# Optimization experiments

Measured on AMD Instinct MI355X. Metric: run time of the kernel, lower is better.

The kernel has to match this reference:

```python
import jax, jax.numpy as jnp
import numpy as np

NUM_ITERS = 2  # quasi-DEER fixed-point iterations (module default num_iters=2)


def _affine_scan(A, b):
    """Parallel first-order linear recurrence h_t = A_t*h_{t-1} + b_t along axis=1.
    A, b: (B, T, H). Equivalent to torch accelerated-scan after removing pow-2 padding."""
    def comb(l, r):
        A1, b1 = l
        A2, b2 = r
        return A2 * A1, A2 * b1 + b2
    return jax.lax.associative_scan(comb, (A, b), axis=1)[1]


def _run_direction(x, W_in, b_in, W_rec, U_z, b_u, num_iters):
    """quasi-DEER evaluation of a MinRNN layer.
    x: (B, T, d_in). Returns states (B, T, H). Initial state h0 = 0 (hx=None)."""
    B, T, _ = x.shape
    H = b_in.shape[0]
    dtype = x.dtype
    h0 = jnp.zeros((B, H), dtype)
    diag_rec = jnp.diagonal(W_rec)  # (H,)
    # z depends only on the input, not on the state -> precompute once.
    z = jnp.tanh(jnp.einsum('bti,hi->bth', x, W_in) + b_in)  # (B, T, H)
    z0, z_rest = z[:, 0], z[:, 1:]
    states = jnp.zeros((B, T, H), dtype)
    for _ in range(num_iters):
        h_prev = states[:, :-1]  # (B, T-1, H), paired with inputs[:,1:]
        u = jax.nn.sigmoid(jnp.einsum('bth,gh->btg', h_prev, W_rec)
                           + jnp.einsum('bth,gh->btg', z_rest, U_z) + b_u)
        fs = u * h_prev + (1.0 - u) * z_rest                      # cell output f
        As = u + (h_prev - z_rest) * u * (1.0 - u) * diag_rec     # diagonal Jacobian
        bs = fs - As * h_prev
        u0 = jax.nn.sigmoid(h0 @ W_rec.T + z0 @ U_z.T + b_u)
        b0 = u0 * h0 + (1.0 - u0) * z0                            # f(x_0, h0)
        A = jnp.concatenate([jnp.zeros_like(b0)[:, None], As], axis=1)  # A0 = 0
        b = jnp.concatenate([b0[:, None], bs], axis=1)
        states = _affine_scan(A, b)
    return states


def _prnn_forward(input, Wf_in, bf_in, Wf_rec, Uf_z, bf_u,
                  Wb_in, bb_in, Wb_rec, Ub_z, bb_u):
    fwd = _run_direction(input, Wf_in, bf_in, Wf_rec, Uf_z, bf_u, NUM_ITERS)
    bwd = _run_direction(input[:, ::-1], Wb_in, bb_in, Wb_rec, Ub_z, bb_u, NUM_ITERS)[:, ::-1]
    output = jnp.concatenate([fwd, bwd], axis=2)      # (B, T, 2H)
    h_n = jnp.stack([fwd[:, -1], bwd[:, 0]])          # (2, B, H)
    return output, h_n


def setup_inputs() -> dict:
    key = jax.random.key(0)
    ks = jax.random.split(key, 12)
    B, T, D_IN, H = 8, 8192, 256, 256
    def minrnn_params(k0, k1, k2, d_in, h):
        kw, kr, ku = k0, k1, k2
        return dict(
            W_in=jax.random.normal(kw, (h, d_in), jnp.float32) / d_in ** 0.5,
            b_in=jnp.zeros((h,), jnp.float32),
            W_rec=jax.random.normal(kr, (h, h), jnp.float32) / h ** 0.5,
            U_z=jax.random.normal(ku, (h, h), jnp.float32) / h ** 0.5,
            b_u=jnp.zeros((h,), jnp.float32),
        )
    pf = minrnn_params(ks[0], ks[1], ks[2], D_IN, H)
    pb = minrnn_params(ks[3], ks[4], ks[5], D_IN, H)
    return {
        'input': jax.random.normal(ks[6], (B, T, D_IN), jnp.float32),
        'Wf_in': pf['W_in'], 'bf_in': pf['b_in'], 'Wf_rec': pf['W_rec'],
        'Uf_z': pf['U_z'], 'bf_u': pf['b_u'],
        'Wb_in': pb['W_in'], 'bb_in': pb['b_in'], 'Wb_rec': pb['W_rec'],
        'Ub_z': pb['U_z'], 'bb_u': pb['b_u'],
    }


def reference(input, Wf_in, bf_in, Wf_rec, Uf_z, bf_u,
              Wb_in, bb_in, Wb_rec, Ub_z, bb_u):
    return _prnn_forward(input, Wf_in, bf_in, Wf_rec, Uf_z, bf_u,
                         Wb_in, bb_in, Wb_rec, Ub_z, bb_u)
```

## Files before the change

### kernel.cpp

```cpp
#include <hip/hip_runtime.h>
#include <stdint.h>

typedef unsigned short u16;
typedef __attribute__((ext_vector_type(8))) short short8v;
typedef __attribute__((ext_vector_type(4))) float f32x4;

#define B_ 8
#define T_ 8192
#define H_ 256
#define M_ 65536
#define MH 16777216
#define NCH 64
#define CHL 128
#define NCHAN 4096

__device__ __forceinline__ u16 f2bf(float f) {
  union { float f; uint32_t u; } v; v.f = f;
  return (u16)((v.u + 0x7FFFu + ((v.u >> 16) & 1u)) >> 16);
}
__device__ __forceinline__ float bf2f(u16 s) {
  union { uint32_t u; float f; } v; v.u = ((uint32_t)s) << 16;
  return v.f;
}
__device__ __forceinline__ float sigm(float x) {
  return __fdividef(1.0f, 1.0f + __expf(-x));
}
__device__ __forceinline__ float tanhfast(float x) {
  return 1.0f - __fdividef(2.0f, __expf(2.0f * x) + 1.0f);
}

__global__ __launch_bounds__(256) void cvt_x_kernel(const float* __restrict__ x,
                                                    u16* __restrict__ xf) {
  size_t i = ((size_t)blockIdx.x * 256 + threadIdx.x) * 8;
  const float4* src = (const float4*)(x + i);
  float4 a = src[0], b = src[1];
  short8v o;
  o[0] = (short)f2bf(a.x); o[1] = (short)f2bf(a.y);
  o[2] = (short)f2bf(a.z); o[3] = (short)f2bf(a.w);
  o[4] = (short)f2bf(b.x); o[5] = (short)f2bf(b.y);
  o[6] = (short)f2bf(b.z); o[7] = (short)f2bf(b.w);
  *(short8v*)(xf + i) = o;
}

__global__ __launch_bounds__(256) void cvt_w_kernel(const float* __restrict__ s0, const float* __restrict__ s1,
                                                    const float* __restrict__ s2, const float* __restrict__ s3,
                                                    const float* __restrict__ s4, const float* __restrict__ s5,
                                                    u16* __restrict__ wbf) {
  int i = blockIdx.x * 256 + threadIdx.x;
  int m = i >> 16, r = i & 65535;
  const float* s = (m == 0) ? s0 : (m == 1) ? s1 : (m == 2) ? s2 : (m == 3) ? s3 : (m == 4) ? s4 : s5;
  wbf[i] = f2bf(s[r]);
}

__device__ __forceinline__ void g2l16(const void* g, void* l) {
  __builtin_amdgcn_global_load_lds((const __attribute__((address_space(1))) void*)g,
                                   (__attribute__((address_space(3))) void*)l, 16, 0, 0);
}

template <int EPI, int REV>
__global__ __launch_bounds__(256) void gemm_k(const u16* __restrict__ A,
                                              const u16* __restrict__ Bw,
                                              const float* __restrict__ bias,
                                              u16* __restrict__ C) {
  __shared__ __align__(16) char ldsA[16384];
  __shared__ __align__(16) char ldsB[16384];
  const int tid = threadIdx.x;
  const int l = tid & 63, w = tid >> 6;
  const int tm = blockIdx.x, tn = blockIdx.y;
  const int m0 = (w >> 1) * 64, n0 = (w & 1) * 64;
  const int wbase = w * 1024;

  f32x4 vzero = {0.f, 0.f, 0.f, 0.f};
  f32x4 acc[4][4];
#pragma unroll
  for (int i = 0; i < 4; ++i)
#pragma unroll
    for (int j = 0; j < 4; ++j) acc[i][j] = vzero;

#pragma unroll
  for (int k0 = 0; k0 < 256; k0 += 64) {
#pragma unroll
    for (int is = 0; is < 4; ++is) {
      const int o = is * 4096 + tid * 16;
      const int row = o >> 7;
      const int cb = o & 127;
      int rA = tm * 128 + row;
      if (REV) { int bb = rA >> 13; int t = rA & 8191; rA = (bb << 13) + (8191 - t); }
      const char* gA = (const char*)A + (size_t)rA * 512 + k0 * 2 + cb;
      g2l16(gA, ldsA + is * 4096 + wbase);
      const int rB = tn * 128 + row;
      const char* gB = (const char*)Bw + (size_t)rB * 512 + k0 * 2 + cb;
      g2l16(gB, ldsB + is * 4096 + wbase);
    }
    __syncthreads();
#pragma unroll
    for (int ks = 0; ks < 2; ++ks) {
      short8v av[4], bv[4];
#pragma unroll
      for (int i = 0; i < 4; ++i) {
        av[i] = *(const short8v*)(ldsA + (m0 + i * 16 + (l & 15)) * 128 + ks * 64 + (l >> 4) * 16);
        bv[i] = *(const short8v*)(ldsB + (n0 + i * 16 + (l & 15)) * 128 + ks * 64 + (l >> 4) * 16);
      }
#pragma unroll
      for (int i = 0; i < 4; ++i)
#pragma unroll
        for (int j = 0; j < 4; ++j)
          acc[i][j] = __builtin_amdgcn_mfma_f32_16x16x32_bf16(av[i], bv[j], acc[i][j], 0, 0, 0);
    }
    __syncthreads();
  }

  const int colb = tn * 128 + n0 + (l & 15);
  const int rowb = tm * 128 + m0 + ((l >> 4) << 2);
#pragma unroll
  for (int j = 0; j < 4; ++j) {
    const int col = colb + j * 16;
    const float bv = (EPI == 2) ? 0.f : bias[col];
#pragma unroll
    for (int i = 0; i < 4; ++i)
#pragma unroll
      for (int r = 0; r < 4; ++r) {
        const int row = rowb + i * 16 + r;
        float xv = acc[i][j][r] + bv;
        if (EPI == 0) xv = tanhfast(xv);
        C[(size_t)row * 256 + col] = f2bf(xv);
      }
  }
}

template <int ITER>
__device__ __forceinline__ void compute_Ab(float zf, float ag, float hp, float dr, bool isT0,
                                           float& Aa, float& bb) {
  const float u = sigm(ag);
  if (isT0) {
    Aa = 0.f; bb = (1.f - u) * zf;
  } else {
    const float g = u * (1.f - u) * dr;
    Aa = u + (hp - zf) * g;
    bb = u * hp + (1.f - u) * zf - Aa * hp;
  }
}

template <int ITER>
__global__ __launch_bounds__(256) void scan_p1_kernel(
    const u16* __restrict__ zb, const u16* __restrict__ zub,
    const u16* __restrict__ s1b, const u16* __restrict__ hw0, const u16* __restrict__ hw1,
    const float* __restrict__ Wf_rec, const float* __restrict__ Wb_rec,
    float* __restrict__ P, float* __restrict__ q) {
  const int wid = blockIdx.x * 4 + (threadIdx.x >> 6);
  const int lane = threadIdx.x & 63;
  const int c = wid & 63;
  int tmp = wid >> 6;
  const int hb = tmp & 3; tmp >>= 2;
  const int b = tmp & 7;
  const int d = tmp >> 3;
  const int h = hb * 64 + lane;
  const float dr = (d ? Wb_rec : Wf_rec)[h * 257];
  const size_t off = ((size_t)b * T_ + (size_t)c * CHL) * H_ + h;
  const u16* zp = zb + (size_t)d * MH + off;
  const u16* zup = zub + (size_t)d * MH + off;
  const u16* s1p = s1b + (size_t)d * MH + off;
  const u16* hwp = (d ? hw1 : hw0) + off;
  const bool chunk0 = (c == 0);
  float Pv = 1.f, qv = 0.f;
#pragma unroll 4
  for (int it = 0; it < CHL; ++it) {
    const size_t ix = (size_t)it * H_;
    float zf = bf2f(zp[ix]);
    float ag = bf2f(zup[ix]);
    float hp = 0.f;
    if (ITER == 2) { ag += bf2f(hwp[ix]); hp = bf2f(s1p[ix]); }
    float Aa, bb;
    compute_Ab<ITER>(zf, ag, hp, dr, chunk0 && it == 0, Aa, bb);
    qv = Aa * qv + bb;
    Pv *= Aa;
  }
  const int ch = (d * 8 + b) * 256 + h;
  P[c * NCHAN + ch] = Pv;
  q[c * NCHAN + ch] = qv;
}

__global__ __launch_bounds__(256) void scan_p2_kernel(const float* __restrict__ P,
                                                      const float* __restrict__ q,
                                                      float* __restrict__ hstart) {
  const int ch = blockIdx.x * 256 + threadIdx.x;
  float hs = 0.f;
#pragma unroll 8
  for (int c = 0; c < NCH; ++c) {
    hstart[c * NCHAN + ch] = hs;
    hs = P[c * NCHAN + ch] * hs + q[c * NCHAN + ch];
  }
}

template <int ITER>
__global__ __launch_bounds__(256) void scan_p3_kernel(
    const u16* __restrict__ zb, const u16* __restrict__ zub,
    const u16* __restrict__ s1b, const u16* __restrict__ hw0, const u16* __restrict__ hw1,
    const float* __restrict__ Wf_rec, const float* __restrict__ Wb_rec,
    const float* __restrict__ hstart,
    u16* __restrict__ s1out, float* __restrict__ out, float* __restrict__ hn) {
  const int wid = blockIdx.x * 4 + (threadIdx.x >> 6);
  const int lane = threadIdx.x & 63;
  const int c = wid & 63;
  int tmp = wid >> 6;
  const int hb = tmp & 3; tmp >>= 2;
  const int b = tmp & 7;
  const int d = tmp >> 3;
  const int h = hb * 64 + lane;
  const float dr = (d ? Wb_rec : Wf_rec)[h * 257];
  const size_t off = ((size_t)b * T_ + (size_t)c * CHL) * H_ + h;
  const u16* zp = zb + (size_t)d * MH + off;
  const u16* zup = zub + (size_t)d * MH + off;
  const u16* s1p = s1b + (size_t)d * MH + off;
  const u16* hwp = (d ? hw1 : hw0) + off;
  const int ch = (d * 8 + b) * 256 + h;
  float hcur = hstart[c * NCHAN + ch];
  if (ITER == 1 && c == 0) {
    s1out[(size_t)d * MH + (size_t)b * T_ * H_ + h] = 0;
  }
  const bool chunk0 = (c == 0);
#pragma unroll 4
  for (int it = 0; it < CHL; ++it) {
    const size_t ix = (size_t)it * H_;
    float zf = bf2f(zp[ix]);
    float ag = bf2f(zup[ix]);
    float hp = 0.f;
    if (ITER == 2) { ag += bf2f(hwp[ix]); hp = bf2f(s1p[ix]); }
    float Aa, bb;
    compute_Ab<ITER>(zf, ag, hp, dr, chunk0 && it == 0, Aa, bb);
    hcur = Aa * hcur + bb;
    const int t = c * CHL + it;
    if (ITER == 1) {
      if (t < T_ - 1)
        s1out[(size_t)d * MH + ((size_t)b * T_ + t + 1) * H_ + h] = f2bf(hcur);
    } else {
      const size_t to = (d == 0) ? ((size_t)b * T_ + t) * 512 + h
                                 : ((size_t)b * T_ + (T_ - 1 - t)) * 512 + 256 + h;
      out[to] = hcur;
      if (t == T_ - 1) hn[(size_t)(d * 8 + b) * 256 + h] = hcur;
    }
  }
}

extern "C" void kernel_launch(void* const* d_in, const int* in_sizes, int n_in,
                              void* d_out, int out_size, void* d_ws, size_t ws_size,
                              hipStream_t stream) {
  const float* x      = (const float*)d_in[0];
  const float* Wf_in  = (const float*)d_in[1];
  const float* bf_in  = (const float*)d_in[2];
  const float* Wf_rec = (const float*)d_in[3];
  const float* Uf_z   = (const float*)d_in[4];
  const float* bf_u   = (const float*)d_in[5];
  const float* Wb_in  = (const float*)d_in[6];
  const float* bb_in  = (const float*)d_in[7];
  const float* Wb_rec = (const float*)d_in[8];
  const float* Ub_z   = (const float*)d_in[9];
  const float* bb_u   = (const float*)d_in[10];

  char* ws = (char*)d_ws;
  const size_t BF = 33554432;
  u16* xf  = (u16*)(ws + 0 * BF);
  u16* z0  = (u16*)(ws + 1 * BF);
  u16* z1  = (u16*)(ws + 2 * BF);
  u16* zu0 = (u16*)(ws + 3 * BF);
  u16* zu1 = (u16*)(ws + 4 * BF);
  u16* s10 = (u16*)(ws + 5 * BF);
  u16* s11 = (u16*)(ws + 6 * BF);
  u16* hw1 = (u16*)(ws + 7 * BF);
  u16* hw0 = xf;
  float* Pbuf = (float*)(ws + 8 * BF);
  float* qbuf = (float*)(ws + 8 * BF + 1048576);
  float* hst  = (float*)(ws + 8 * BF + 2097152);
  u16* wbf    = (u16*)(ws + 8 * BF + 3145728);
  (void)ws_size; (void)in_sizes; (void)n_in; (void)out_size;

  float* outp = (float*)d_out;
  float* hnp  = outp + (size_t)33554432;

  dim3 gg(512, 2, 1);

  cvt_x_kernel<<<8192, 256, 0, stream>>>(x, xf);
  cvt_w_kernel<<<1536, 256, 0, stream>>>(Wf_in, Uf_z, Wf_rec, Wb_in, Ub_z, Wb_rec, wbf);

  gemm_k<0, 0><<<gg, 256, 0, stream>>>(xf, wbf + 0 * 65536, bf_in, z0);
  gemm_k<0, 1><<<gg, 256, 0, stream>>>(xf, wbf + 3 * 65536, bb_in, z1);
  gemm_k<1, 0><<<gg, 256, 0, stream>>>(z0, wbf + 1 * 65536, bf_u, zu0);
  gemm_k<1, 0><<<gg, 256, 0, stream>>>(z1, wbf + 4 * 65536, bb_u, zu1);

  scan_p1_kernel<1><<<1024, 256, 0, stream>>>(z0, zu0, s10, hw0, hw1, Wf_rec, Wb_rec, Pbuf, qbuf);
  scan_p2_kernel<<<16, 256, 0, stream>>>(Pbuf, qbuf, hst);
  scan_p3_kernel<1><<<1024, 256, 0, stream>>>(z0, zu0, s10, hw0, hw1, Wf_rec, Wb_rec, hst,
                                              s10, nullptr, nullptr);

  gemm_k<2, 0><<<gg, 256, 0, stream>>>(s10, wbf + 2 * 65536, nullptr, hw0);
  gemm_k<2, 0><<<gg, 256, 0, stream>>>(s11, wbf + 5 * 65536, nullptr, hw1);

  scan_p1_kernel<2><<<1024, 256, 0, stream>>>(z0, zu0, s10, hw0, hw1, Wf_rec, Wb_rec, Pbuf, qbuf);
  scan_p2_kernel<<<16, 256, 0, stream>>>(Pbuf, qbuf, hst);
  scan_p3_kernel<2><<<1024, 256, 0, stream>>>(z0, zu0, s10, hw0, hw1, Wf_rec, Wb_rec, hst,
                                              nullptr, outp, hnp);
}
```

Before: 400.9 us.

## Fuse recurrent GEMM into zu buffer and vectorize scans over four channels

The recurrent-weight GEMM now adds its result directly into the precomputed zu pre-activation buffer, so the second-iteration scans no longer read a separate hw buffer. Scan kernels process four contiguous hidden channels per lane with vector bf16 loads and float4 stores. Chunks are shortened to 32 steps, with 256 chunks. The t=0 special case is removed, relying on zero initial state. The trade-off is a longer serial chunk-carry pass and an extra read in the GEMM epilogue.

```diff
diff --git a/kernel.cpp b/kernel.cpp
--- a/kernel.cpp
+++ b/kernel.cpp
@@ -3,6 +3,7 @@
 
 typedef unsigned short u16;
 typedef __attribute__((ext_vector_type(8))) short short8v;
+typedef __attribute__((ext_vector_type(4))) short short4v;
 typedef __attribute__((ext_vector_type(4))) float f32x4;
 
 #define B_ 8
@@ -10,8 +11,8 @@
 #define H_ 256
 #define M_ 65536
 #define MH 16777216
-#define NCH 64
-#define CHL 128
+#define NCH 256
+#define CHL 32
 #define NCHAN 4096
 
 __device__ __forceinline__ u16 f2bf(float f) {
@@ -61,7 +62,8 @@
 __global__ __launch_bounds__(256) void gemm_k(const u16* __restrict__ A,
                                               const u16* __restrict__ Bw,
                                               const float* __restrict__ bias,
-                                              u16* __restrict__ C) {
+                                              const u16* addm,
+                                              u16* C) {
   __shared__ __align__(16) char ldsA[16384];
   __shared__ __align__(16) char ldsB[16384];
   const int tid = threadIdx.x;
@@ -115,69 +117,71 @@
 #pragma unroll
   for (int j = 0; j < 4; ++j) {
     const int col = colb + j * 16;
-    const float bv = (EPI == 2) ? 0.f : bias[col];
+    const float bv = (EPI == 3) ? 0.f : bias[col];
 #pragma unroll
     for (int i = 0; i < 4; ++i)
 #pragma unroll
       for (int r = 0; r < 4; ++r) {
         const int row = rowb + i * 16 + r;
         float xv = acc[i][j][r] + bv;
+        if (EPI == 3) xv += bf2f(addm[(size_t)row * 256 + col]);
         if (EPI == 0) xv = tanhfast(xv);
         C[(size_t)row * 256 + col] = f2bf(xv);
       }
   }
 }
 
-template <int ITER>
-__device__ __forceinline__ void compute_Ab(float zf, float ag, float hp, float dr, bool isT0,
+__device__ __forceinline__ void compute_Ab(float zf, float ag, float hp, float dr,
                                            float& Aa, float& bb) {
   const float u = sigm(ag);
-  if (isT0) {
-    Aa = 0.f; bb = (1.f - u) * zf;
-  } else {
-    const float g = u * (1.f - u) * dr;
-    Aa = u + (hp - zf) * g;
-    bb = u * hp + (1.f - u) * zf - Aa * hp;
-  }
+  const float g = u * (1.f - u) * dr;
+  Aa = u + (hp - zf) * g;
+  bb = u * hp + (1.f - u) * zf - Aa * hp;
 }
 
 template <int ITER>
 __global__ __launch_bounds__(256) void scan_p1_kernel(
     const u16* __restrict__ zb, const u16* __restrict__ zub,
-    const u16* __restrict__ s1b, const u16* __restrict__ hw0, const u16* __restrict__ hw1,
+    const u16* __restrict__ s1b,
     const float* __restrict__ Wf_rec, const float* __restrict__ Wb_rec,
     float* __restrict__ P, float* __restrict__ q) {
   const int wid = blockIdx.x * 4 + (threadIdx.x >> 6);
   const int lane = threadIdx.x & 63;
-  const int c = wid & 63;
-  int tmp = wid >> 6;
-  const int hb = tmp & 3; tmp >>= 2;
+  const int c = wid & (NCH - 1);
+  const int tmp = wid >> 8;
   const int b = tmp & 7;
   const int d = tmp >> 3;
-  const int h = hb * 64 + lane;
-  const float dr = (d ? Wb_rec : Wf_rec)[h * 257];
-  const size_t off = ((size_t)b * T_ + (size_t)c * CHL) * H_ + h;
-  const u16* zp = zb + (size_t)d * MH + off;
-  const u16* zup = zub + (size_t)d * MH + off;
-  const u16* s1p = s1b + (size_t)d * MH + off;
-  const u16* hwp = (d ? hw1 : hw0) + off;
-  const bool chunk0 = (c == 0);
-  float Pv = 1.f, qv = 0.f;
+  const int h0 = lane * 4;
+  const float* Wr = d ? Wb_rec : Wf_rec;
+  float dr[4];
+#pragma unroll
+  for (int j = 0; j < 4; ++j) dr[j] = Wr[(h0 + j) * 257];
+  const size_t off = (size_t)d * MH + ((size_t)b * T_ + (size_t)c * CHL) * H_ + h0;
+  const u16* zp = zb + off;
+  const u16* zup = zub + off;
+  const u16* s1p = s1b + off;
+  float Pv[4] = {1.f, 1.f, 1.f, 1.f}, qv[4] = {0.f, 0.f, 0.f, 0.f};
 #pragma unroll 4
   for (int it = 0; it < CHL; ++it) {
     const size_t ix = (size_t)it * H_;
-    float zf = bf2f(zp[ix]);
-    float ag = bf2f(zup[ix]);
-    float hp = 0.f;
-    if (ITER == 2) { ag += bf2f(hwp[ix]); hp = bf2f(s1p[ix]); }
-    float Aa, bb;
-    compute_Ab<ITER>(zf, ag, hp, dr, chunk0 && it == 0, Aa, bb);
-    qv = Aa * qv + bb;
-    Pv *= Aa;
-  }
-  const int ch = (d * 8 + b) * 256 + h;
-  P[c * NCHAN + ch] = Pv;
-  q[c * NCHAN + ch] = qv;
+    short4v z4 = *(const short4v*)(zp + ix);
+    short4v a4 = *(const short4v*)(zup + ix);
+    short4v s4 = {0, 0, 0, 0};
+    if (ITER == 2) s4 = *(const short4v*)(s1p + ix);
+#pragma unroll
+    for (int j = 0; j < 4; ++j) {
+      const float zf = bf2f((u16)z4[j]);
+      const float ag = bf2f((u16)a4[j]);
+      const float hp = (ITER == 2) ? bf2f((u16)s4[j]) : 0.f;
+      float Aa, bb;
+      compute_Ab(zf, ag, hp, dr[j], Aa, bb);
+      qv[j] = Aa * qv[j] + bb;
+      Pv[j] *= Aa;
+    }
+  }
+  const int ch0 = (d * 8 + b) * 256 + h0;
+  *(f32x4*)(P + (size_t)c * NCHAN + ch0) = (f32x4){Pv[0], Pv[1], Pv[2], Pv[3]};
+  *(f32x4*)(q + (size_t)c * NCHAN + ch0) = (f32x4){qv[0], qv[1], qv[2], qv[3]};
 }
 
 __global__ __launch_bounds__(256) void scan_p2_kernel(const float* __restrict__ P,
@@ -195,49 +199,60 @@
 template <int ITER>
 __global__ __launch_bounds__(256) void scan_p3_kernel(
     const u16* __restrict__ zb, const u16* __restrict__ zub,
-    const u16* __restrict__ s1b, const u16* __restrict__ hw0, const u16* __restrict__ hw1,
+    const u16* __restrict__ s1b,
     const float* __restrict__ Wf_rec, const float* __restrict__ Wb_rec,
     const float* __restrict__ hstart,
     u16* __restrict__ s1out, float* __restrict__ out, float* __restrict__ hn) {
   const int wid = blockIdx.x * 4 + (threadIdx.x >> 6);
   const int lane = threadIdx.x & 63;
-  const int c = wid & 63;
-  int tmp = wid >> 6;
-  const int hb = tmp & 3; tmp >>= 2;
+  const int c = wid & (NCH - 1);
+  const int tmp = wid >> 8;
   const int b = tmp & 7;
   const int d = tmp >> 3;
-  const int h = hb * 64 + lane;
-  const float dr = (d ? Wb_rec : Wf_rec)[h * 257];
-  const size_t off = ((size_t)b * T_ + (size_t)c * CHL) * H_ + h;
-  const u16* zp = zb + (size_t)d * MH + off;
-  const u16* zup = zub + (size_t)d * MH + off;
-  const u16* s1p = s1b + (size_t)d * MH + off;
-  const u16* hwp = (d ? hw1 : hw0) + off;
-  const int ch = (d * 8 + b) * 256 + h;
-  float hcur = hstart[c * NCHAN + ch];
+  const int h0 = lane * 4;
+  const float* Wr = d ? Wb_rec : Wf_rec;
+  float dr[4];
+#pragma unroll
+  for (int j = 0; j < 4; ++j) dr[j] = Wr[(h0 + j) * 257];
+  const size_t off = (size_t)d * MH + ((size_t)b * T_ + (size_t)c * CHL) * H_ + h0;
+  const u16* zp = zb + off;
+  const u16* zup = zub + off;
+  const u16* s1p = s1b + off;
+  const int ch0 = (d * 8 + b) * 256 + h0;
+  f32x4 h4 = *(const f32x4*)(hstart + (size_t)c * NCHAN + ch0);
+  float hc[4] = {h4[0], h4[1], h4[2], h4[3]};
   if (ITER == 1 && c == 0) {
-    s1out[(size_t)d * MH + (size_t)b * T_ * H_ + h] = 0;
-  }
-  const bool chunk0 = (c == 0);
+    *(short4v*)(s1out + off) = (short4v){0, 0, 0, 0};
+  }
 #pragma unroll 4
   for (int it = 0; it < CHL; ++it) {
     const size_t ix = (size_t)it * H_;
-    float zf = bf2f(zp[ix]);
-    float ag = bf2f(zup[ix]);
-    float hp = 0.f;
-    if (ITER == 2) { ag += bf2f(hwp[ix]); hp = bf2f(s1p[ix]); }
-    float Aa, bb;
-    compute_Ab<ITER>(zf, ag, hp, dr, chunk0 && it == 0, Aa, bb);
-    hcur = Aa * hcur + bb;
+    short4v z4 = *(const short4v*)(zp + ix);
+    short4v a4 = *(const short4v*)(zup + ix);
+    short4v s4 = {0, 0, 0, 0};
+    if (ITER == 2) s4 = *(const short4v*)(s1p + ix);
+#pragma unroll
+    for (int j = 0; j < 4; ++j) {
+      const float zf = bf2f((u16)z4[j]);
+      const float ag = bf2f((u16)a4[j]);
+      const float hp = (ITER == 2) ? bf2f((u16)s4[j]) : 0.f;
+      float Aa, bb;
+      compute_Ab(zf, ag, hp, dr[j], Aa, bb);
+      hc[j] = Aa * hc[j] + bb;
+    }
     const int t = c * CHL + it;
     if (ITER == 1) {
-      if (t < T_ - 1)
-        s1out[(size_t)d * MH + ((size_t)b * T_ + t + 1) * H_ + h] = f2bf(hcur);
+      if (t < T_ - 1) {
+        short4v o = {(short)f2bf(hc[0]), (short)f2bf(hc[1]),
+                     (short)f2bf(hc[2]), (short)f2bf(hc[3])};
+        *(short4v*)(s1out + off + ix + H_) = o;
+      }
     } else {
-      const size_t to = (d == 0) ? ((size_t)b * T_ + t) * 512 + h
-                                 : ((size_t)b * T_ + (T_ - 1 - t)) * 512 + 256 + h;
-      out[to] = hcur;
-      if (t == T_ - 1) hn[(size_t)(d * 8 + b) * 256 + h] = hcur;
+      const size_t to = (d == 0) ? ((size_t)b * T_ + t) * 512 + h0
+                                 : ((size_t)b * T_ + (T_ - 1 - t)) * 512 + 256 + h0;
+      *(f32x4*)(out + to) = (f32x4){hc[0], hc[1], hc[2], hc[3]};
+      if (t == T_ - 1)
+        *(f32x4*)(hn + (size_t)(d * 8 + b) * 256 + h0) = (f32x4){hc[0], hc[1], hc[2], hc[3]};
     }
   }
 }
@@ -266,12 +281,10 @@
   u16* zu1 = (u16*)(ws + 4 * BF);
   u16* s10 = (u16*)(ws + 5 * BF);
   u16* s11 = (u16*)(ws + 6 * BF);
-  u16* hw1 = (u16*)(ws + 7 * BF);
-  u16* hw0 = xf;
-  float* Pbuf = (float*)(ws + 8 * BF);
-  float* qbuf = (float*)(ws + 8 * BF + 1048576);
-  float* hst  = (float*)(ws + 8 * BF + 2097152);
-  u16* wbf    = (u16*)(ws + 8 * BF + 3145728);
+  u16* wbf    = (u16*)(ws + 7 * BF);
+  float* Pbuf = (float*)(ws + 7 * BF + 786432);
+  float* qbuf = (float*)(ws + 7 * BF + 786432 + 4194304);
+  float* hst  = (float*)(ws + 7 * BF + 786432 + 8388608);
   (void)ws_size; (void)in_sizes; (void)n_in; (void)out_size;
 
   float* outp = (float*)d_out;
@@ -282,21 +295,21 @@
   cvt_x_kernel<<<8192, 256, 0, stream>>>(x, xf);
   cvt_w_kernel<<<1536, 256, 0, stream>>>(Wf_in, Uf_z, Wf_rec, Wb_in, Ub_z, Wb_rec, wbf);
 
-  gemm_k<0, 0><<<gg, 256, 0, stream>>>(xf, wbf + 0 * 65536, bf_in, z0);
-  gemm_k<0, 1><<<gg, 256, 0, stream>>>(xf, wbf + 3 * 65536, bb_in, z1);
-  gemm_k<1, 0><<<gg, 256, 0, stream>>>(z0, wbf + 1 * 65536, bf_u, zu0);
-  gemm_k<1, 0><<<gg, 256, 0, stream>>>(z1, wbf + 4 * 65536, bb_u, zu1);
-
-  scan_p1_kernel<1><<<1024, 256, 0, stream>>>(z0, zu0, s10, hw0, hw1, Wf_rec, Wb_rec, Pbuf, qbuf);
+  gemm_k<0, 0><<<gg, 256, 0, stream>>>(xf, wbf + 0 * 65536, bf_in, nullptr, z0);
+  gemm_k<0, 1><<<gg, 256, 0, stream>>>(xf, wbf + 3 * 65536, bb_in, nullptr, z1);
+  gemm_k<1, 0><<<gg, 256, 0, stream>>>(z0, wbf + 1 * 65536, bf_u, nullptr, zu0);
+  gemm_k<1, 0><<<gg, 256, 0, stream>>>(z1, wbf + 4 * 65536, bb_u, nullptr, zu1);
+
+  scan_p1_kernel<1><<<1024, 256, 0, stream>>>(z0, zu0, s10, Wf_rec, Wb_rec, Pbuf, qbuf);
   scan_p2_kernel<<<16, 256, 0, stream>>>(Pbuf, qbuf, hst);
-  scan_p3_kernel<1><<<1024, 256, 0, stream>>>(z0, zu0, s10, hw0, hw1, Wf_rec, Wb_rec, hst,
+  scan_p3_kernel<1><<<1024, 256, 0, stream>>>(z0, zu0, s10, Wf_rec, Wb_rec, hst,
                                               s10, nullptr, nullptr);
 
-  gemm_k<2, 0><<<gg, 256, 0, stream>>>(s10, wbf + 2 * 65536, nullptr, hw0);
-  gemm_k<2, 0><<<gg, 256, 0, stream>>>(s11, wbf + 5 * 65536, nullptr, hw1);
-
-  scan_p1_kernel<2><<<1024, 256, 0, stream>>>(z0, zu0, s10, hw0, hw1, Wf_rec, Wb_rec, Pbuf, qbuf);
+  gemm_k<3, 0><<<gg, 256, 0, stream>>>(s10, wbf + 2 * 65536, nullptr, zu0, zu0);
+  gemm_k<3, 0><<<gg, 256, 0, stream>>>(s11, wbf + 5 * 65536, nullptr, zu1, zu1);
+
+  scan_p1_kernel<2><<<1024, 256, 0, stream>>>(z0, zu0, s10, Wf_rec, Wb_rec, Pbuf, qbuf);
   scan_p2_kernel<<<16, 256, 0, stream>>>(Pbuf, qbuf, hst);
-  scan_p3_kernel<2><<<1024, 256, 0, stream>>>(z0, zu0, s10, hw0, hw1, Wf_rec, Wb_rec, hst,
+  scan_p3_kernel<2><<<1024, 256, 0, stream>>>(z0, zu0, s10, Wf_rec, Wb_rec, hst,
                                               nullptr, outp, hnp);
 }
```

New measurement: 404.3 us. No clear change (+0.8%).
